# Kernel optimization log

Measured on AMD Instinct MI355X. Metric: run time of the kernel, lower is better.

Reference implementation:

```python
import jax, jax.numpy as jnp
import numpy as np

E = 300000        # num_edges
T = 3000000       # num_triplets
D = 128           # edge_message_dim
N_RAD = 6
N_SPH = 7
D_DOWN = 64       # edge_down_dim
D_BAS = 8         # basis_embed_dim


def _w(key, fan_in, fan_out):
    return jax.random.normal(key, (fan_in, fan_out), jnp.float32) / np.sqrt(fan_in)


def setup_inputs() -> dict:
    key = jax.random.key(0)
    ks = jax.random.split(key, 32)
    inp = {
        "x": jax.random.normal(ks[0], (E, D), jnp.float32),
        "rbf": jax.random.uniform(ks[1], (E, N_RAD), jnp.float32),
        "sbf": jax.random.uniform(ks[2], (T, N_SPH * N_RAD), jnp.float32),
        "idx_kj": jax.random.randint(ks[3], (T,), 0, E),
        "idx_ji": jax.random.randint(ks[4], (T,), 0, E),
        # basis projections (bias-free)
        "w_rbf1": _w(ks[5], N_RAD, D_BAS),
        "w_rbf2": _w(ks[6], D_BAS, D),
        "w_sbf1": _w(ks[7], N_SPH * N_RAD, D_BAS),
        "w_sbf2": _w(ks[8], D_BAS, D_DOWN),
        # message linears (with bias)
        "w_kj": _w(ks[9], D, D), "b_kj": jnp.zeros((D,), jnp.float32),
        "w_ji": _w(ks[10], D, D), "b_ji": jnp.zeros((D,), jnp.float32),
        # down / up projections (bias-free)
        "w_down": _w(ks[11], D, D_DOWN),
        "w_up": _w(ks[12], D_DOWN, D),
        # residual block before skip + dense
        "res1_w1": _w(ks[13], D, D), "res1_b1": jnp.zeros((D,), jnp.float32),
        "res1_w2": _w(ks[14], D, D), "res1_b2": jnp.zeros((D,), jnp.float32),
        "w_bs": _w(ks[15], D, D), "b_bs": jnp.zeros((D,), jnp.float32),
        # two residual blocks after skip
        "res2_w1": _w(ks[16], D, D), "res2_b1": jnp.zeros((D,), jnp.float32),
        "res2_w2": _w(ks[17], D, D), "res2_b2": jnp.zeros((D,), jnp.float32),
        "res3_w1": _w(ks[18], D, D), "res3_b1": jnp.zeros((D,), jnp.float32),
        "res3_w2": _w(ks[19], D, D), "res3_b2": jnp.zeros((D,), jnp.float32),
    }
    return inp


def _res_block(h, w1, b1, w2, b2):
    # h + act(lin2(act(lin1(h)))) with Swish(beta=1) == silu
    return h + jax.nn.silu(jax.nn.silu(h @ w1 + b1) @ w2 + b2)


def reference(x, rbf, sbf, idx_kj, idx_ji,
              w_rbf1, w_rbf2, w_sbf1, w_sbf2,
              w_kj, b_kj, w_ji, b_ji, w_down, w_up,
              res1_w1, res1_b1, res1_w2, res1_b2, w_bs, b_bs,
              res2_w1, res2_b1, res2_w2, res2_b2,
              res3_w1, res3_b1, res3_w2, res3_b2):
    act = jax.nn.silu
    x_ji = act(x @ w_ji + b_ji)                       # [E, D]
    x_kj = act(x @ w_kj + b_kj)                       # [E, D]
    rbf_e = (rbf @ w_rbf1) @ w_rbf2                   # [E, D]
    x_kj = act((x_kj * rbf_e) @ w_down)               # [E, D_DOWN]
    sbf_e = (sbf @ w_sbf1) @ w_sbf2                   # [T, D_DOWN]
    m = x_kj[idx_kj] * sbf_e                          # gather + Hadamard [T, D_DOWN]
    agg = jax.ops.segment_sum(m, idx_ji, num_segments=x.shape[0])  # [E, D_DOWN]
    x_kj = act(agg @ w_up)                            # [E, D]
    h = _res_block(x_ji + x_kj, res1_w1, res1_b1, res1_w2, res1_b2)
    h = act(h @ w_bs + b_bs) + x                      # skip connection
    h = _res_block(h, res2_w1, res2_b1, res2_w2, res2_b2)
    h = _res_block(h, res3_w1, res3_b1, res3_w2, res3_b2)
    return h
```

## Files before the change

### kernel.cpp

```cpp
#include <hip/hip_runtime.h>
#include <hip/hip_bf16.h>


typedef __attribute__((ext_vector_type(8))) _Float16 f16x8;
typedef __attribute__((ext_vector_type(4))) float f32x4;

__device__ __forceinline__ float silu_f(float v) {
    return v * __builtin_amdgcn_rcpf(1.0f + __expf(-v));
}

__device__ __forceinline__ void split44h(f32x4 a, f32x4 b, f16x8& hi, f16x8& lo) {
    float f[8] = {a[0], a[1], a[2], a[3], b[0], b[1], b[2], b[3]};
    #pragma unroll
    for (int j = 0; j < 8; ++j) {
        const _Float16 h = (_Float16)f[j];
        hi[j] = h;
        lo[j] = (_Float16)(f[j] - (float)h);
    }
}

__device__ __forceinline__ void gll16(const void* g, void* l) {
    __builtin_amdgcn_global_load_lds((const __attribute__((address_space(1))) void*)g,
                                     (__attribute__((address_space(3))) void*)l, 16, 0, 0);
}
__device__ __forceinline__ void stage8k(const char* g, _Float16* l, int lane, int wid) {
    #pragma unroll
    for (int i = 0; i < 2; ++i) {
        const int off = ((i * 4 + wid) << 10);
        gll16(g + off + lane * 16, (char*)l + off);
    }
}
__device__ __forceinline__ void stage4k(const char* g, _Float16* l, int lane, int wid) {
    const int off = (wid << 10);
    gll16(g + off + lane * 16, (char*)l + off);
}

template<int NF>
__device__ __forceinline__ void mfma_ks(f16x8 ah, f16x8 al, const _Float16* slot,
                                        int acol, int kq, f32x4* acc) {
    #pragma unroll
    for (int n = 0; n < NF; ++n) {
        const int c = n * 16 + acol;
        const int sw = (kq ^ ((c >> 1) & 3)) << 3;
        const f16x8 bh = *(const f16x8*)&slot[c * 32 + sw];
        acc[n] = __builtin_amdgcn_mfma_f32_16x16x32_f16(ah, bh, acc[n], 0, 0, 0);
        acc[n] = __builtin_amdgcn_mfma_f32_16x16x32_f16(al, bh, acc[n], 0, 0, 0);
    }
}

__device__ __forceinline__ void tfrag(const float* tl, int rb, int q, int kq,
                                      f16x8& Ah, f16x8& Al) {
    const f32x4 ta = *(const f32x4*)&tl[rb + q * 32 + kq * 8];
    const f32x4 tb = *(const f32x4*)&tl[rb + q * 32 + kq * 8 + 4];
    split44h(ta, tb, Ah, Al);
}

__device__ __forceinline__ void tgemm4(const char* img, const char* imgnext,
                                       _Float16* sA, _Float16* sB, const float* tl, int rb,
                                       int kq, int acol, int lane, int wid, f32x4* acc)
{
    f16x8 Ah[4], Al[4];
    #pragma unroll
    for (int q = 0; q < 4; ++q) tfrag(tl, rb, q, kq, Ah[q], Al[q]);

    stage8k(img + 8192, sB, lane, wid);
    mfma_ks<8>(Ah[0], Al[0], sA, acol, kq, acc); __syncthreads();
    stage8k(img + 16384, sA, lane, wid);
    mfma_ks<8>(Ah[1], Al[1], sB, acol, kq, acc); __syncthreads();
    stage8k(img + 24576, sB, lane, wid);
    mfma_ks<8>(Ah[2], Al[2], sA, acol, kq, acc); __syncthreads();
    if (imgnext) stage8k(imgnext, sA, lane, wid);
    mfma_ks<8>(Ah[3], Al[3], sB, acol, kq, acc); __syncthreads();
}

#define TPITCH 132

struct WDesc { const float* src; char* dst; int K; int N; };
struct WPrepArgs { WDesc w[11]; };

__global__ void wprep_kernel(WPrepArgs args) {
    const WDesc d = args.w[blockIdx.y];
    const int h = blockIdx.x;
    if (h * 32 >= d.K) return;
    char* slab = d.dst + (size_t)h * d.N * 64;
    for (int idx = threadIdx.x; idx < d.N * 4; idx += 256) {
        const int c = idx >> 2, ch = idx & 3;
        f16x8 v;
        #pragma unroll
        for (int j = 0; j < 8; ++j)
            v[j] = (_Float16)d.src[(size_t)(h * 32 + ch * 8 + j) * d.N + c];
        *(f16x8*)(slab + c * 64 + ((ch ^ ((c >> 1) & 3)) << 4)) = v;
    }
}


__global__ void rbf1_kernel(const float* __restrict__ rbf, const float* __restrict__ w_rbf1,
                            float* __restrict__ re1, int E) {
    const int i = blockIdx.x * 256 + threadIdx.x;
    const int e = i >> 3, p = i & 7;
    if (e < E) {
        float s = 0.f;
        #pragma unroll
        for (int q = 0; q < 6; ++q) s = fmaf(rbf[e * 6 + q], w_rbf1[q * 8 + p], s);
        re1[i] = s;
    }
}

__global__ void count_rank_kernel(const int* __restrict__ idx_ji, int* __restrict__ cnt,
                                  int* __restrict__ rank, int T) {
    const int i = (blockIdx.x * 256 + threadIdx.x) * 4;
    if (i + 3 < T) {
        const int4 j = *(const int4*)&idx_ji[i];
        int4 r;
        r.x = atomicAdd(&cnt[j.x], 1);
        r.y = atomicAdd(&cnt[j.y], 1);
        r.z = atomicAdd(&cnt[j.z], 1);
        r.w = atomicAdd(&cnt[j.w], 1);
        *(int4*)&rank[i] = r;
    } else {
        for (int k = i; k < T; ++k) rank[k] = atomicAdd(&cnt[idx_ji[k]], 1);
    }
}

__global__ void scan_partial_kernel(const int* __restrict__ cnt, int* __restrict__ partial, int E) {
    __shared__ int red[256];
    const int tid = threadIdx.x;
    const int base = blockIdx.x * 1024 + tid * 4;
    int s = 0;
    #pragma unroll
    for (int i = 0; i < 4; ++i) { const int g = base + i; if (g < E) s += cnt[g]; }
    red[tid] = s;
    __syncthreads();
    for (int off = 128; off > 0; off >>= 1) {
        if (tid < off) red[tid] += red[tid + off];
        __syncthreads();
    }
    if (tid == 0) partial[blockIdx.x] = red[0];
}

__global__ void scan_block_kernel(const int* __restrict__ partial, int* __restrict__ blockoff,
                                  int NB, int* offsets, int E) {
    __shared__ int red[256];
    const int tid = threadIdx.x;
    int v[4]; int s = 0;
    #pragma unroll
    for (int i = 0; i < 4; ++i) { const int g = tid * 4 + i; v[i] = (g < NB) ? partial[g] : 0; s += v[i]; }
    red[tid] = s;
    __syncthreads();
    for (int off = 1; off < 256; off <<= 1) {
        const int add = (tid >= off) ? red[tid - off] : 0;
        __syncthreads();
        red[tid] += add;
        __syncthreads();
    }
    int excl = (tid == 0) ? 0 : red[tid - 1];
    #pragma unroll
    for (int i = 0; i < 4; ++i) { const int g = tid * 4 + i; if (g < NB) blockoff[g] = excl; excl += v[i]; }
    if (tid == 255) offsets[E] = red[255];
}

__global__ void scan_final_kernel(const int* __restrict__ cnt, const int* __restrict__ blockoff,
                                  int* __restrict__ offsets, int E) {
    __shared__ int red[256];
    const int tid = threadIdx.x;
    const int base = blockIdx.x * 1024 + tid * 4;
    int v[4]; int s = 0;
    #pragma unroll
    for (int i = 0; i < 4; ++i) { const int g = base + i; v[i] = (g < E) ? cnt[g] : 0; s += v[i]; }
    red[tid] = s;
    __syncthreads();
    for (int off = 1; off < 256; off <<= 1) {
        const int add = (tid >= off) ? red[tid - off] : 0;
        __syncthreads();
        red[tid] += add;
        __syncthreads();
    }
    int run = blockoff[blockIdx.x] + ((tid == 0) ? 0 : red[tid - 1]);
    #pragma unroll
    for (int i = 0; i < 4; ++i) {
        const int g = base + i;
        if (g < E) offsets[g] = run;
        run += v[i];
    }
}

__launch_bounds__(256, 3)
__global__ void e1fill_kernel(const float* __restrict__ sbf, const float* __restrict__ w_sbf1,
                              const int* __restrict__ idx_ji, const int* __restrict__ idx_kj,
                              const int* __restrict__ rank, const int* __restrict__ offsets,
                              _Float16* __restrict__ E1p, int* __restrict__ kjp, int T)
{
    __shared__ float s_lds[256 * 43];
    const int tid = threadIdx.x;
    const long long t0 = (long long)blockIdx.x * 256;
    const int nrow = min(256, (int)(T - t0));
    const int nel  = nrow * 42;
    const float* base = sbf + t0 * 42;

    for (int i = tid * 4; i + 3 < nel; i += 1024) {
        const float4 v = *(const float4*)&base[i];
        s_lds[(i + 0) + (i + 0) / 42] = v.x;
        s_lds[(i + 1) + (i + 1) / 42] = v.y;
        s_lds[(i + 2) + (i + 2) / 42] = v.z;
        s_lds[(i + 3) + (i + 3) / 42] = v.w;
    }
    const int tail0 = nel & ~3;
    if (tid < nel - tail0) { const int g = tail0 + tid; s_lds[g + g / 42] = base[g]; }
    __syncthreads();

    const int t = (int)t0 + tid;
    if (t >= T) return;
    const float* srow = &s_lds[tid * 43];
    float e1[8] = {0.f, 0.f, 0.f, 0.f, 0.f, 0.f, 0.f, 0.f};
    #pragma unroll
    for (int q = 0; q < 42; ++q) {
        const float s = srow[q];
        #pragma unroll
        for (int p = 0; p < 8; ++p) e1[p] = fmaf(s, w_sbf1[q * 8 + p], e1[p]);
    }
    f16x8 eh;
    #pragma unroll
    for (int p = 0; p < 8; ++p) eh[p] = (_Float16)e1[p];
    const int ji  = idx_ji[t];
    const int pos = offsets[ji] + rank[t];
    *(f16x8*)&E1p[(size_t)pos * 8] = eh;
    kjp[pos] = idx_kj[t];
}

__launch_bounds__(256, 4)
__global__ void gather_kernel(const _Float16* __restrict__ E1p, const int* __restrict__ kjp,
                              const float* __restrict__ w_sbf2, const int* __restrict__ offsets,
                              const _Float16* __restrict__ xkjd, float* __restrict__ agg, int E)
{
    const int tid  = threadIdx.x;
    const int lane = tid & 63;
    const int e    = blockIdx.x * 4 + (tid >> 6);

    float w2[8];
    #pragma unroll
    for (int p = 0; p < 8; ++p) w2[p] = w_sbf2[p * 64 + lane];

    if (e >= E) return;
    const int j0 = __builtin_amdgcn_readfirstlane(offsets[e]);
    const int j1 = __builtin_amdgcn_readfirstlane(offsets[e + 1]);

    float acc = 0.f;
    if (j0 < j1) {
        int kj = __builtin_amdgcn_readfirstlane(kjp[j0]);
        f16x8 ev = *(const f16x8*)&E1p[(size_t)j0 * 8];
        float xv = (float)xkjd[(size_t)kj * 64 + lane];
        for (int j = j0; j < j1; ++j) {
            float xn = 0.f; f16x8 evn = {};
            if (j + 1 < j1) {
                const int kn = __builtin_amdgcn_readfirstlane(kjp[j + 1]);
                evn = *(const f16x8*)&E1p[(size_t)(j + 1) * 8];
                xn  = (float)xkjd[(size_t)kn * 64 + lane];
            }
            float sv = (float)ev[0] * w2[0];
            sv = fmaf((float)ev[1], w2[1], sv);
            sv = fmaf((float)ev[2], w2[2], sv);
            sv = fmaf((float)ev[3], w2[3], sv);
            sv = fmaf((float)ev[4], w2[4], sv);
            sv = fmaf((float)ev[5], w2[5], sv);
            sv = fmaf((float)ev[6], w2[6], sv);
            sv = fmaf((float)ev[7], w2[7], sv);
            acc = fmaf(xv, sv, acc);
            ev = evn; xv = xn;
        }
    }
    agg[(size_t)e * 64 + lane] = acc;
}

__launch_bounds__(256, 3)
__global__ void k1_kernel(const float* __restrict__ x, const char* __restrict__ wkj_i,
                          const float* __restrict__ b_kj, const float* __restrict__ re1,
                          const float* __restrict__ w_rbf2, const char* __restrict__ wdn_i,
                          _Float16* __restrict__ W3, int E)
{
    __shared__ _Float16 slotA[4096], slotB[4096];
    __shared__ float t_lds[64 * TPITCH];
    __shared__ float w2_lds[8 * 128];
    const int tid = threadIdx.x, lane = tid & 63, wid = tid >> 6;
    const int acol = lane & 15, kq = lane >> 4;
    const int rowW = blockIdx.x * 64 + wid * 16;
    const int arow = rowW + acol;
    const bool av = arow < E;

    stage8k(wkj_i, slotA, lane, wid);
    const float* xr = x + (size_t)arow * 128;
    f16x8 aH[4], aL[4];
    #pragma unroll
    for (int ks = 0; ks < 4; ++ks) {
        f32x4 a0 = f32x4{0.f, 0.f, 0.f, 0.f}, a1 = f32x4{0.f, 0.f, 0.f, 0.f};
        if (av) { a0 = *(const f32x4*)&xr[ks * 32 + kq * 8];
                  a1 = *(const f32x4*)&xr[ks * 32 + kq * 8 + 4]; }
        split44h(a0, a1, aH[ks], aL[ks]);
    }
    float bv[8];
    #pragma unroll
    for (int n = 0; n < 8; ++n) bv[n] = b_kj[n * 16 + acol];
    f32x4 e1a[4], e1b[4];
    #pragma unroll
    for (int r = 0; r < 4; ++r) {
        const int ge = rowW + kq * 4 + r;
        e1a[r] = f32x4{0.f, 0.f, 0.f, 0.f}; e1b[r] = f32x4{0.f, 0.f, 0.f, 0.f};
        if (ge < E) { e1a[r] = *(const f32x4*)&re1[(size_t)ge * 8];
                      e1b[r] = *(const f32x4*)&re1[(size_t)ge * 8 + 4]; }
    }
    for (int i = tid; i < 1024; i += 256) w2_lds[i] = w_rbf2[i];
    __syncthreads();

    f32x4 acc[8];
    #pragma unroll
    for (int n = 0; n < 8; ++n) acc[n] = f32x4{0.f, 0.f, 0.f, 0.f};

    stage8k(wkj_i + 8192, slotB, lane, wid);
    mfma_ks<8>(aH[0], aL[0], slotA, acol, kq, acc); __syncthreads();
    stage8k(wkj_i + 16384, slotA, lane, wid);
    mfma_ks<8>(aH[1], aL[1], slotB, acol, kq, acc); __syncthreads();
    stage8k(wkj_i + 24576, slotB, lane, wid);
    mfma_ks<8>(aH[2], aL[2], slotA, acol, kq, acc); __syncthreads();
    stage4k(wdn_i, slotA, lane, wid);
    mfma_ks<8>(aH[3], aL[3], slotB, acol, kq, acc); __syncthreads();

    #pragma unroll
    for (int n = 0; n < 8; ++n) {
        const int c = n * 16 + acol;
        float w2c[8];
        #pragma unroll
        for (int p = 0; p < 8; ++p) w2c[p] = w2_lds[p * 128 + c];
        #pragma unroll
        for (int r = 0; r < 4; ++r) {
            float s = e1a[r][0] * w2c[0];
            s = fmaf(e1a[r][1], w2c[1], s);
            s = fmaf(e1a[r][2], w2c[2], s);
            s = fmaf(e1a[r][3], w2c[3], s);
            s = fmaf(e1b[r][0], w2c[4], s);
            s = fmaf(e1b[r][1], w2c[5], s);
            s = fmaf(e1b[r][2], w2c[6], s);
            s = fmaf(e1b[r][3], w2c[7], s);
            t_lds[(wid * 16 + kq * 4 + r) * TPITCH + c] = silu_f(acc[n][r] + bv[n]) * s;
        }
    }
    __syncthreads();

    f32x4 acc2[4];
    #pragma unroll
    for (int n = 0; n < 4; ++n) acc2[n] = f32x4{0.f, 0.f, 0.f, 0.f};
    const int rb = (wid * 16 + acol) * TPITCH;

    f16x8 tH[4], tL[4];
    #pragma unroll
    for (int q = 0; q < 4; ++q) tfrag(t_lds, rb, q, kq, tH[q], tL[q]);

    stage4k(wdn_i + 4096, slotB, lane, wid);
    mfma_ks<4>(tH[0], tL[0], slotA, acol, kq, acc2); __syncthreads();
    stage4k(wdn_i + 8192, slotA, lane, wid);
    mfma_ks<4>(tH[1], tL[1], slotB, acol, kq, acc2); __syncthreads();
    stage4k(wdn_i + 12288, slotB, lane, wid);
    mfma_ks<4>(tH[2], tL[2], slotA, acol, kq, acc2); __syncthreads();
    mfma_ks<4>(tH[3], tL[3], slotB, acol, kq, acc2);

    #pragma unroll
    for (int n = 0; n < 4; ++n) {
        const int c = n * 16 + acol;
        #pragma unroll
        for (int r = 0; r < 4; ++r) {
            const int ge = rowW + kq * 4 + r;
            if (ge < E) W3[(size_t)ge * 64 + c] = (_Float16)silu_f(acc2[n][r]);
        }
    }
}

struct KBigArgs {
    const float* x; const float* W4; float* out;
    const char *wji, *wup, *r1w1, *r1w2, *wbs, *r2w1, *r2w2, *r3w1, *r3w2;
    const float *bji, *r1b1, *r1b2, *bbs, *r2b1, *r2b2, *r3b1, *r3b2;
    int E;
};

__launch_bounds__(256, 3)
__global__ void kbig_kernel(KBigArgs A_)
{
    __shared__ _Float16 slotA[4096], slotB[4096];
    __shared__ float t_lds[64 * TPITCH];
    const int tid = threadIdx.x, lane = tid & 63, wid = tid >> 6;
    const int acol = lane & 15, kq = lane >> 4;
    const int rowW = blockIdx.x * 64 + wid * 16;
    const int arow = rowW + acol;
    const int E = A_.E;
    const bool av = arow < E;
    const int rb = (wid * 16 + acol) * TPITCH;

    stage8k(A_.wji, slotA, lane, wid);

    const float* xr = A_.x + (size_t)arow * 128;
    const float* wr = A_.W4 + (size_t)arow * 64;
    f16x8 aH[4], aL[4], uH[2], uL[2];
    #pragma unroll
    for (int ks = 0; ks < 4; ++ks) {
        f32x4 a0 = f32x4{0.f, 0.f, 0.f, 0.f}, a1 = f32x4{0.f, 0.f, 0.f, 0.f};
        if (av) { a0 = *(const f32x4*)&xr[ks * 32 + kq * 8];
                  a1 = *(const f32x4*)&xr[ks * 32 + kq * 8 + 4]; }
        split44h(a0, a1, aH[ks], aL[ks]);
    }
    #pragma unroll
    for (int ks = 0; ks < 2; ++ks) {
        f32x4 u0 = f32x4{0.f, 0.f, 0.f, 0.f}, u1 = f32x4{0.f, 0.f, 0.f, 0.f};
        if (av) { u0 = *(const f32x4*)&wr[ks * 32 + kq * 8];
                  u1 = *(const f32x4*)&wr[ks * 32 + kq * 8 + 4]; }
        split44h(u0, u1, uH[ks], uL[ks]);
    }
    __syncthreads();

    f32x4 acc[8];
    #pragma unroll
    for (int n = 0; n < 8; ++n) acc[n] = f32x4{0.f, 0.f, 0.f, 0.f};

    stage8k(A_.wji + 8192, slotB, lane, wid);
    mfma_ks<8>(aH[0], aL[0], slotA, acol, kq, acc); __syncthreads();
    stage8k(A_.wji + 16384, slotA, lane, wid);
    mfma_ks<8>(aH[1], aL[1], slotB, acol, kq, acc); __syncthreads();
    stage8k(A_.wji + 24576, slotB, lane, wid);
    mfma_ks<8>(aH[2], aL[2], slotA, acol, kq, acc); __syncthreads();
    stage8k(A_.wup, slotA, lane, wid);
    mfma_ks<8>(aH[3], aL[3], slotB, acol, kq, acc); __syncthreads();

    float res[8][4];
    #pragma unroll
    for (int n = 0; n < 8; ++n) {
        const float bv = A_.bji[n * 16 + acol];
        #pragma unroll
        for (int r = 0; r < 4; ++r) { res[n][r] = silu_f(acc[n][r] + bv); acc[n][r] = 0.f; }
    }

    stage8k(A_.wup + 8192, slotB, lane, wid);
    mfma_ks<8>(uH[0], uL[0], slotA, acol, kq, acc); __syncthreads();
    stage8k(A_.r1w1, slotA, lane, wid);
    mfma_ks<8>(uH[1], uL[1], slotB, acol, kq, acc); __syncthreads();

    #pragma unroll
    for (int n = 0; n < 8; ++n) {
        const int c = n * 16 + acol;
        #pragma unroll
        for (int r = 0; r < 4; ++r) {
            res[n][r] += silu_f(acc[n][r]);
            t_lds[(wid * 16 + kq * 4 + r) * TPITCH + c] = res[n][r];
            acc[n][r] = 0.f;
        }
    }
    __syncthreads();

    tgemm4(A_.r1w1, A_.r1w2, slotA, slotB, t_lds, rb, kq, acol, lane, wid, acc);
    #pragma unroll
    for (int n = 0; n < 8; ++n) {
        const float bv = A_.r1b1[n * 16 + acol];
        const int c = n * 16 + acol;
        #pragma unroll
        for (int r = 0; r < 4; ++r) {
            t_lds[(wid * 16 + kq * 4 + r) * TPITCH + c] = silu_f(acc[n][r] + bv);
            acc[n][r] = 0.f;
        }
    }
    __syncthreads();

    tgemm4(A_.r1w2, A_.wbs, slotA, slotB, t_lds, rb, kq, acol, lane, wid, acc);
    #pragma unroll
    for (int n = 0; n < 8; ++n) {
        const float bv = A_.r1b2[n * 16 + acol];
        const int c = n * 16 + acol;
        #pragma unroll
        for (int r = 0; r < 4; ++r) {
            t_lds[(wid * 16 + kq * 4 + r) * TPITCH + c] = res[n][r] + silu_f(acc[n][r] + bv);
            acc[n][r] = 0.f;
        }
    }
    __syncthreads();

    tgemm4(A_.wbs, A_.r2w1, slotA, slotB, t_lds, rb, kq, acol, lane, wid, acc);
    #pragma unroll
    for (int n = 0; n < 8; ++n) {
        const float bv = A_.bbs[n * 16 + acol];
        const int c = n * 16 + acol;
        #pragma unroll
        for (int r = 0; r < 4; ++r) {
            const int ge = rowW + kq * 4 + r;
            const float xv = (ge < E) ? A_.x[(size_t)ge * 128 + c] : 0.f;
            res[n][r] = silu_f(acc[n][r] + bv) + xv;
            t_lds[(wid * 16 + kq * 4 + r) * TPITCH + c] = res[n][r];
            acc[n][r] = 0.f;
        }
    }
    __syncthreads();

    tgemm4(A_.r2w1, A_.r2w2, slotA, slotB, t_lds, rb, kq, acol, lane, wid, acc);
    #pragma unroll
    for (int n = 0; n < 8; ++n) {
        const float bv = A_.r2b1[n * 16 + acol];
        const int c = n * 16 + acol;
        #pragma unroll
        for (int r = 0; r < 4; ++r) {
            t_lds[(wid * 16 + kq * 4 + r) * TPITCH + c] = silu_f(acc[n][r] + bv);
            acc[n][r] = 0.f;
        }
    }
    __syncthreads();

    tgemm4(A_.r2w2, A_.r3w1, slotA, slotB, t_lds, rb, kq, acol, lane, wid, acc);
    #pragma unroll
    for (int n = 0; n < 8; ++n) {
        const float bv = A_.r2b2[n * 16 + acol];
        const int c = n * 16 + acol;
        #pragma unroll
        for (int r = 0; r < 4; ++r) {
            res[n][r] += silu_f(acc[n][r] + bv);
            t_lds[(wid * 16 + kq * 4 + r) * TPITCH + c] = res[n][r];
            acc[n][r] = 0.f;
        }
    }
    __syncthreads();

    tgemm4(A_.r3w1, A_.r3w2, slotA, slotB, t_lds, rb, kq, acol, lane, wid, acc);
    #pragma unroll
    for (int n = 0; n < 8; ++n) {
        const float bv = A_.r3b1[n * 16 + acol];
        const int c = n * 16 + acol;
        #pragma unroll
        for (int r = 0; r < 4; ++r) {
            t_lds[(wid * 16 + kq * 4 + r) * TPITCH + c] = silu_f(acc[n][r] + bv);
            acc[n][r] = 0.f;
        }
    }
    __syncthreads();

    tgemm4(A_.r3w2, nullptr, slotA, slotB, t_lds, rb, kq, acol, lane, wid, acc);
    #pragma unroll
    for (int n = 0; n < 8; ++n) {
        const float bv = A_.r3b2[n * 16 + acol];
        const int c = n * 16 + acol;
        #pragma unroll
        for (int r = 0; r < 4; ++r) {
            const int ge = rowW + kq * 4 + r;
            if (ge < E)
                A_.out[(size_t)ge * 128 + c] = res[n][r] + silu_f(acc[n][r] + bv);
        }
    }
}


extern "C" void kernel_launch(void* const* d_in, const int* in_sizes, int n_in,
                              void* d_out, int out_size, void* d_ws, size_t ws_size,
                              hipStream_t stream)
{
    const float* x      = (const float*)d_in[0];
    const float* rbf    = (const float*)d_in[1];
    const float* sbf    = (const float*)d_in[2];
    const int*   idx_kj = (const int*)d_in[3];
    const int*   idx_ji = (const int*)d_in[4];
    const float* w_rbf1 = (const float*)d_in[5];
    const float* w_rbf2 = (const float*)d_in[6];
    const float* w_sbf1 = (const float*)d_in[7];
    const float* w_sbf2 = (const float*)d_in[8];
    const float* w_kj   = (const float*)d_in[9];
    const float* b_kj   = (const float*)d_in[10];
    const float* w_ji   = (const float*)d_in[11];
    const float* b_ji   = (const float*)d_in[12];
    const float* w_down = (const float*)d_in[13];
    const float* w_up   = (const float*)d_in[14];
    const float* r1w1   = (const float*)d_in[15];
    const float* r1b1   = (const float*)d_in[16];
    const float* r1w2   = (const float*)d_in[17];
    const float* r1b2   = (const float*)d_in[18];
    const float* w_bs   = (const float*)d_in[19];
    const float* b_bs   = (const float*)d_in[20];
    const float* r2w1   = (const float*)d_in[21];
    const float* r2b1   = (const float*)d_in[22];
    const float* r2w2   = (const float*)d_in[23];
    const float* r2b2   = (const float*)d_in[24];
    const float* r3w1   = (const float*)d_in[25];
    const float* r3b1   = (const float*)d_in[26];
    const float* r3w2   = (const float*)d_in[27];
    const float* r3b2   = (const float*)d_in[28];

    const int E = in_sizes[0] / 128;
    const int T = in_sizes[2] / 42;

    float* OUT = (float*)d_out;
    _Float16* W3 = (_Float16*)((char*)d_ws + (size_t)E * 128 * 4);
    float* W4  = (float*)((char*)d_ws + (size_t)E * 128 * 4
                                      + (size_t)E * 64 * 4);

    int*   cnt      = (int*)d_ws;
    int*   offsets  = cnt + (E + 64);
    int*   partial  = offsets + (E + 64);
    int*   blockoff = partial + 1024;
    _Float16* E1p   = (_Float16*)((char*)d_ws + (4u << 20));
    int*   kjp      = (int*)((char*)d_ws + (102u << 20));
    float* re1      = (float*)((char*)d_ws + (116u << 20));
    char*  wimg     = (char*)d_ws + (130u << 20);
    int*   rank     = (int*)((char*)d_ws + (134u << 20));

    char* wkj_i  = wimg;
    char* wji_i  = wimg + 32768;
    char* wdn_i  = wimg + 65536;
    char* wup_i  = wimg + 81920;
    char* r1w1_i = wimg + 98304;
    char* r1w2_i = wimg + 131072;
    char* wbs_i  = wimg + 163840;
    char* r2w1_i = wimg + 196608;
    char* r2w2_i = wimg + 229376;
    char* r3w1_i = wimg + 262144;
    char* r3w2_i = wimg + 294912;

    WPrepArgs pa;
    pa.w[0]  = {w_kj,   wkj_i,  128, 128};
    pa.w[1]  = {w_ji,   wji_i,  128, 128};
    pa.w[2]  = {w_down, wdn_i,  128,  64};
    pa.w[3]  = {w_up,   wup_i,   64, 128};
    pa.w[4]  = {r1w1,   r1w1_i, 128, 128};
    pa.w[5]  = {r1w2,   r1w2_i, 128, 128};
    pa.w[6]  = {w_bs,   wbs_i,  128, 128};
    pa.w[7]  = {r2w1,   r2w1_i, 128, 128};
    pa.w[8]  = {r2w2,   r2w2_i, 128, 128};
    pa.w[9]  = {r3w1,   r3w1_i, 128, 128};
    pa.w[10] = {r3w2,   r3w2_i, 128, 128};

    const dim3 b256(256);
    const int gB  = (E + 63) / 64;
    const int gT  = (T + 255) / 256;
    const int gT4 = (T + 1023) / 1024;
    const int NB  = (E + 1023) / 1024;
    const int gE4 = (E + 3) / 4;
    const int gR  = (E * 8 + 255) / 256;

    wprep_kernel<<<dim3(4, 11), b256, 0, stream>>>(pa);
    rbf1_kernel<<<gR, b256, 0, stream>>>(rbf, w_rbf1, re1, E);
    hipMemsetAsync(cnt, 0, (size_t)E * 4, stream);
    count_rank_kernel<<<gT4, b256, 0, stream>>>(idx_ji, cnt, rank, T);
    scan_partial_kernel<<<NB, b256, 0, stream>>>(cnt, partial, E);
    scan_block_kernel<<<1, b256, 0, stream>>>(partial, blockoff, NB, offsets, E);
    scan_final_kernel<<<NB, b256, 0, stream>>>(cnt, blockoff, offsets, E);
    e1fill_kernel<<<gT, b256, 0, stream>>>(sbf, w_sbf1, idx_ji, idx_kj, rank, offsets, E1p, kjp, T);

    k1_kernel<<<gB, b256, 0, stream>>>(x, wkj_i, b_kj, re1, w_rbf2, wdn_i, W3, E);
    gather_kernel<<<gE4, b256, 0, stream>>>(E1p, kjp, w_sbf2, offsets, W3, W4, E);

    KBigArgs ka;
    ka.x = x; ka.W4 = W4; ka.out = OUT;
    ka.wji = wji_i; ka.wup = wup_i; ka.r1w1 = r1w1_i; ka.r1w2 = r1w2_i; ka.wbs = wbs_i;
    ka.r2w1 = r2w1_i; ka.r2w2 = r2w2_i; ka.r3w1 = r3w1_i; ka.r3w2 = r3w2_i;
    ka.bji = b_ji; ka.r1b1 = r1b1; ka.r1b2 = r1b2; ka.bbs = b_bs;
    ka.r2b1 = r2b1; ka.r2b2 = r2b2; ka.r3b1 = r3b1; ka.r3b2 = r3b2;
    ka.E = E;
    kbig_kernel<<<gB, b256, 0, stream>>>(ka);
}
```

Baseline: 999.0 us.

## Merge independent prologue kernels and co-schedule k1 with e1fill in one launch

```diff
diff --git a/kernel.cpp b/kernel.cpp
--- a/kernel.cpp
+++ b/kernel.cpp
@@ -74,13 +74,19 @@
 }
 
 #define TPITCH 132
+#define SMEM_K1 54272
 
 struct WDesc { const float* src; char* dst; int K; int N; };
-struct WPrepArgs { WDesc w[11]; };
-
-__global__ void wprep_kernel(WPrepArgs args) {
-    const WDesc d = args.w[blockIdx.y];
-    const int h = blockIdx.x;
+struct ProArgs {
+    WDesc w[11];
+    const float* rbf; const float* w_rbf1; float* re1; int E;
+    const int* idx_ji; int* cnt; int* rank; int T;
+    int nW, nR;
+};
+
+__device__ void wprep_body(const ProArgs& P, int b) {
+    const WDesc d = P.w[b >> 2];
+    const int h = b & 3;
     if (h * 32 >= d.K) return;
     char* slab = d.dst + (size_t)h * d.N * 64;
     for (int idx = threadIdx.x; idx < d.N * 4; idx += 256) {
@@ -93,34 +99,40 @@
     }
 }
 
-
-__global__ void rbf1_kernel(const float* __restrict__ rbf, const float* __restrict__ w_rbf1,
-                            float* __restrict__ re1, int E) {
-    const int i = blockIdx.x * 256 + threadIdx.x;
+__device__ void rbf1_body(const ProArgs& P, int b) {
+    const int i = b * 256 + threadIdx.x;
     const int e = i >> 3, p = i & 7;
-    if (e < E) {
+    if (e < P.E) {
         float s = 0.f;
         #pragma unroll
-        for (int q = 0; q < 6; ++q) s = fmaf(rbf[e * 6 + q], w_rbf1[q * 8 + p], s);
-        re1[i] = s;
-    }
-}
-
-__global__ void count_rank_kernel(const int* __restrict__ idx_ji, int* __restrict__ cnt,
-                                  int* __restrict__ rank, int T) {
-    const int i = (blockIdx.x * 256 + threadIdx.x) * 4;
+        for (int q = 0; q < 6; ++q) s = fmaf(P.rbf[e * 6 + q], P.w_rbf1[q * 8 + p], s);
+        P.re1[i] = s;
+    }
+}
+
+__device__ void count_rank_body(const ProArgs& P, int b) {
+    const int i = (b * 256 + threadIdx.x) * 4;
+    const int T = P.T;
     if (i + 3 < T) {
-        const int4 j = *(const int4*)&idx_ji[i];
+        const int4 j = *(const int4*)&P.idx_ji[i];
         int4 r;
-        r.x = atomicAdd(&cnt[j.x], 1);
-        r.y = atomicAdd(&cnt[j.y], 1);
-        r.z = atomicAdd(&cnt[j.z], 1);
-        r.w = atomicAdd(&cnt[j.w], 1);
-        *(int4*)&rank[i] = r;
+        r.x = atomicAdd(&P.cnt[j.x], 1);
+        r.y = atomicAdd(&P.cnt[j.y], 1);
+        r.z = atomicAdd(&P.cnt[j.z], 1);
+        r.w = atomicAdd(&P.cnt[j.w], 1);
+        *(int4*)&P.rank[i] = r;
     } else {
-        for (int k = i; k < T; ++k) rank[k] = atomicAdd(&cnt[idx_ji[k]], 1);
-    }
-}
+        for (int k = i; k < T; ++k) P.rank[k] = atomicAdd(&P.cnt[P.idx_ji[k]], 1);
+    }
+}
+
+__global__ void pro_kernel(ProArgs P) {
+    const int b = blockIdx.x;
+    if (b < P.nW)            wprep_body(P, b);
+    else if (b < P.nW + P.nR) rbf1_body(P, b - P.nW);
+    else                      count_rank_body(P, b - P.nW - P.nR);
+}
+
 
 __global__ void scan_partial_kernel(const int* __restrict__ cnt, int* __restrict__ partial, int E) {
     __shared__ int red[256];
@@ -184,18 +196,120 @@
     }
 }
 
-__launch_bounds__(256, 3)
-__global__ void e1fill_kernel(const float* __restrict__ sbf, const float* __restrict__ w_sbf1,
-                              const int* __restrict__ idx_ji, const int* __restrict__ idx_kj,
-                              const int* __restrict__ rank, const int* __restrict__ offsets,
-                              _Float16* __restrict__ E1p, int* __restrict__ kjp, int T)
-{
-    __shared__ float s_lds[256 * 43];
+struct K1E1Args {
+    const float* x; const char* wkj_i; const float* b_kj; const float* re1;
+    const float* w_rbf2; const char* wdn_i; _Float16* W3; int E; int gB;
+    const float* sbf; const float* w_sbf1;
+    const int* idx_ji; const int* idx_kj; const int* rank; const int* offsets;
+    _Float16* E1p; int* kjp; int T;
+};
+
+__device__ void k1_body(char* smem, int bx, const K1E1Args& A) {
+    _Float16* slotA = (_Float16*)smem;
+    _Float16* slotB = (_Float16*)(smem + 8192);
+    float* t_lds    = (float*)(smem + 16384);
+    float* w2_lds   = (float*)(smem + 16384 + 64 * TPITCH * 4);
+    const int tid = threadIdx.x, lane = tid & 63, wid = tid >> 6;
+    const int acol = lane & 15, kq = lane >> 4;
+    const int rowW = bx * 64 + wid * 16;
+    const int arow = rowW + acol;
+    const int E = A.E;
+    const bool av = arow < E;
+
+    stage8k(A.wkj_i, slotA, lane, wid);
+    const float* xr = A.x + (size_t)arow * 128;
+    f16x8 aH[4], aL[4];
+    #pragma unroll
+    for (int ks = 0; ks < 4; ++ks) {
+        f32x4 a0 = f32x4{0.f, 0.f, 0.f, 0.f}, a1 = f32x4{0.f, 0.f, 0.f, 0.f};
+        if (av) { a0 = *(const f32x4*)&xr[ks * 32 + kq * 8];
+                  a1 = *(const f32x4*)&xr[ks * 32 + kq * 8 + 4]; }
+        split44h(a0, a1, aH[ks], aL[ks]);
+    }
+    float bv[8];
+    #pragma unroll
+    for (int n = 0; n < 8; ++n) bv[n] = A.b_kj[n * 16 + acol];
+    f32x4 e1a[4], e1b[4];
+    #pragma unroll
+    for (int r = 0; r < 4; ++r) {
+        const int ge = rowW + kq * 4 + r;
+        e1a[r] = f32x4{0.f, 0.f, 0.f, 0.f}; e1b[r] = f32x4{0.f, 0.f, 0.f, 0.f};
+        if (ge < E) { e1a[r] = *(const f32x4*)&A.re1[(size_t)ge * 8];
+                      e1b[r] = *(const f32x4*)&A.re1[(size_t)ge * 8 + 4]; }
+    }
+    for (int i = tid; i < 1024; i += 256) w2_lds[i] = A.w_rbf2[i];
+    __syncthreads();
+
+    f32x4 acc[8];
+    #pragma unroll
+    for (int n = 0; n < 8; ++n) acc[n] = f32x4{0.f, 0.f, 0.f, 0.f};
+
+    stage8k(A.wkj_i + 8192, slotB, lane, wid);
+    mfma_ks<8>(aH[0], aL[0], slotA, acol, kq, acc); __syncthreads();
+    stage8k(A.wkj_i + 16384, slotA, lane, wid);
+    mfma_ks<8>(aH[1], aL[1], slotB, acol, kq, acc); __syncthreads();
+    stage8k(A.wkj_i + 24576, slotB, lane, wid);
+    mfma_ks<8>(aH[2], aL[2], slotA, acol, kq, acc); __syncthreads();
+    stage4k(A.wdn_i, slotA, lane, wid);
+    mfma_ks<8>(aH[3], aL[3], slotB, acol, kq, acc); __syncthreads();
+
+    #pragma unroll
+    for (int n = 0; n < 8; ++n) {
+        const int c = n * 16 + acol;
+        float w2c[8];
+        #pragma unroll
+        for (int p = 0; p < 8; ++p) w2c[p] = w2_lds[p * 128 + c];
+        #pragma unroll
+        for (int r = 0; r < 4; ++r) {
+            float s = e1a[r][0] * w2c[0];
+            s = fmaf(e1a[r][1], w2c[1], s);
+            s = fmaf(e1a[r][2], w2c[2], s);
+            s = fmaf(e1a[r][3], w2c[3], s);
+            s = fmaf(e1b[r][0], w2c[4], s);
+            s = fmaf(e1b[r][1], w2c[5], s);
+            s = fmaf(e1b[r][2], w2c[6], s);
+            s = fmaf(e1b[r][3], w2c[7], s);
+            t_lds[(wid * 16 + kq * 4 + r) * TPITCH + c] = silu_f(acc[n][r] + bv[n]) * s;
+        }
+    }
+    __syncthreads();
+
+    f32x4 acc2[4];
+    #pragma unroll
+    for (int n = 0; n < 4; ++n) acc2[n] = f32x4{0.f, 0.f, 0.f, 0.f};
+    const int rb = (wid * 16 + acol) * TPITCH;
+
+    f16x8 tH[4], tL[4];
+    #pragma unroll
+    for (int q = 0; q < 4; ++q) tfrag(t_lds, rb, q, kq, tH[q], tL[q]);
+
+    stage4k(A.wdn_i + 4096, slotB, lane, wid);
+    mfma_ks<4>(tH[0], tL[0], slotA, acol, kq, acc2); __syncthreads();
+    stage4k(A.wdn_i + 8192, slotA, lane, wid);
+    mfma_ks<4>(tH[1], tL[1], slotB, acol, kq, acc2); __syncthreads();
+    stage4k(A.wdn_i + 12288, slotB, lane, wid);
+    mfma_ks<4>(tH[2], tL[2], slotA, acol, kq, acc2); __syncthreads();
+    mfma_ks<4>(tH[3], tL[3], slotB, acol, kq, acc2);
+
+    #pragma unroll
+    for (int n = 0; n < 4; ++n) {
+        const int c = n * 16 + acol;
+        #pragma unroll
+        for (int r = 0; r < 4; ++r) {
+            const int ge = rowW + kq * 4 + r;
+            if (ge < E) A.W3[(size_t)ge * 64 + c] = (_Float16)silu_f(acc2[n][r]);
+        }
+    }
+}
+
+__device__ void e1fill_body(char* smem, int bx, const K1E1Args& A) {
+    float* s_lds = (float*)smem;
     const int tid = threadIdx.x;
-    const long long t0 = (long long)blockIdx.x * 256;
+    const int T = A.T;
+    const long long t0 = (long long)bx * 256;
     const int nrow = min(256, (int)(T - t0));
     const int nel  = nrow * 42;
-    const float* base = sbf + t0 * 42;
+    const float* base = A.sbf + t0 * 42;
 
     for (int i = tid * 4; i + 3 < nel; i += 1024) {
         const float4 v = *(const float4*)&base[i];
@@ -216,15 +330,23 @@
     for (int q = 0; q < 42; ++q) {
         const float s = srow[q];
         #pragma unroll
-        for (int p = 0; p < 8; ++p) e1[p] = fmaf(s, w_sbf1[q * 8 + p], e1[p]);
+        for (int p = 0; p < 8; ++p) e1[p] = fmaf(s, A.w_sbf1[q * 8 + p], e1[p]);
     }
     f16x8 eh;
     #pragma unroll
     for (int p = 0; p < 8; ++p) eh[p] = (_Float16)e1[p];
-    const int ji  = idx_ji[t];
-    const int pos = offsets[ji] + rank[t];
-    *(f16x8*)&E1p[(size_t)pos * 8] = eh;
-    kjp[pos] = idx_kj[t];
+    const int ji  = A.idx_ji[t];
+    const int pos = A.offsets[ji] + A.rank[t];
+    *(f16x8*)&A.E1p[(size_t)pos * 8] = eh;
+    A.kjp[pos] = A.idx_kj[t];
+}
+
+__launch_bounds__(256, 2)
+__global__ void k1e1_kernel(K1E1Args A) {
+    __shared__ __align__(16) char smem[SMEM_K1];
+    const int b = blockIdx.x;
+    if (b < A.gB) k1_body(smem, b, A);
+    else          e1fill_body(smem, b - A.gB, A);
 }
 
 __launch_bounds__(256, 4)
@@ -269,107 +391,6 @@
         }
     }
     agg[(size_t)e * 64 + lane] = acc;
-}
-
-__launch_bounds__(256, 3)
-__global__ void k1_kernel(const float* __restrict__ x, const char* __restrict__ wkj_i,
-                          const float* __restrict__ b_kj, const float* __restrict__ re1,
-                          const float* __restrict__ w_rbf2, const char* __restrict__ wdn_i,
-                          _Float16* __restrict__ W3, int E)
-{
-    __shared__ _Float16 slotA[4096], slotB[4096];
-    __shared__ float t_lds[64 * TPITCH];
-    __shared__ float w2_lds[8 * 128];
-    const int tid = threadIdx.x, lane = tid & 63, wid = tid >> 6;
-    const int acol = lane & 15, kq = lane >> 4;
-    const int rowW = blockIdx.x * 64 + wid * 16;
-    const int arow = rowW + acol;
-    const bool av = arow < E;
-
-    stage8k(wkj_i, slotA, lane, wid);
-    const float* xr = x + (size_t)arow * 128;
-    f16x8 aH[4], aL[4];
-    #pragma unroll
-    for (int ks = 0; ks < 4; ++ks) {
-        f32x4 a0 = f32x4{0.f, 0.f, 0.f, 0.f}, a1 = f32x4{0.f, 0.f, 0.f, 0.f};
-        if (av) { a0 = *(const f32x4*)&xr[ks * 32 + kq * 8];
-                  a1 = *(const f32x4*)&xr[ks * 32 + kq * 8 + 4]; }
-        split44h(a0, a1, aH[ks], aL[ks]);
-    }
-    float bv[8];
-    #pragma unroll
-    for (int n = 0; n < 8; ++n) bv[n] = b_kj[n * 16 + acol];
-    f32x4 e1a[4], e1b[4];
-    #pragma unroll
-    for (int r = 0; r < 4; ++r) {
-        const int ge = rowW + kq * 4 + r;
-        e1a[r] = f32x4{0.f, 0.f, 0.f, 0.f}; e1b[r] = f32x4{0.f, 0.f, 0.f, 0.f};
-        if (ge < E) { e1a[r] = *(const f32x4*)&re1[(size_t)ge * 8];
-                      e1b[r] = *(const f32x4*)&re1[(size_t)ge * 8 + 4]; }
-    }
-    for (int i = tid; i < 1024; i += 256) w2_lds[i] = w_rbf2[i];
-    __syncthreads();
-
-    f32x4 acc[8];
-    #pragma unroll
-    for (int n = 0; n < 8; ++n) acc[n] = f32x4{0.f, 0.f, 0.f, 0.f};
-
-    stage8k(wkj_i + 8192, slotB, lane, wid);
-    mfma_ks<8>(aH[0], aL[0], slotA, acol, kq, acc); __syncthreads();
-    stage8k(wkj_i + 16384, slotA, lane, wid);
-    mfma_ks<8>(aH[1], aL[1], slotB, acol, kq, acc); __syncthreads();
-    stage8k(wkj_i + 24576, slotB, lane, wid);
-    mfma_ks<8>(aH[2], aL[2], slotA, acol, kq, acc); __syncthreads();
-    stage4k(wdn_i, slotA, lane, wid);
-    mfma_ks<8>(aH[3], aL[3], slotB, acol, kq, acc); __syncthreads();
-
-    #pragma unroll
-    for (int n = 0; n < 8; ++n) {
-        const int c = n * 16 + acol;
-        float w2c[8];
-        #pragma unroll
-        for (int p = 0; p < 8; ++p) w2c[p] = w2_lds[p * 128 + c];
-        #pragma unroll
-        for (int r = 0; r < 4; ++r) {
-            float s = e1a[r][0] * w2c[0];
-            s = fmaf(e1a[r][1], w2c[1], s);
-            s = fmaf(e1a[r][2], w2c[2], s);
-            s = fmaf(e1a[r][3], w2c[3], s);
-            s = fmaf(e1b[r][0], w2c[4], s);
-            s = fmaf(e1b[r][1], w2c[5], s);
-            s = fmaf(e1b[r][2], w2c[6], s);
-            s = fmaf(e1b[r][3], w2c[7], s);
-            t_lds[(wid * 16 + kq * 4 + r) * TPITCH + c] = silu_f(acc[n][r] + bv[n]) * s;
-        }
-    }
-    __syncthreads();
-
-    f32x4 acc2[4];
-    #pragma unroll
-    for (int n = 0; n < 4; ++n) acc2[n] = f32x4{0.f, 0.f, 0.f, 0.f};
-    const int rb = (wid * 16 + acol) * TPITCH;
-
-    f16x8 tH[4], tL[4];
-    #pragma unroll
-    for (int q = 0; q < 4; ++q) tfrag(t_lds, rb, q, kq, tH[q], tL[q]);
-
-    stage4k(wdn_i + 4096, slotB, lane, wid);
-    mfma_ks<4>(tH[0], tL[0], slotA, acol, kq, acc2); __syncthreads();
-    stage4k(wdn_i + 8192, slotA, lane, wid);
-    mfma_ks<4>(tH[1], tL[1], slotB, acol, kq, acc2); __syncthreads();
-    stage4k(wdn_i + 12288, slotB, lane, wid);
-    mfma_ks<4>(tH[2], tL[2], slotA, acol, kq, acc2); __syncthreads();
-    mfma_ks<4>(tH[3], tL[3], slotB, acol, kq, acc2);
-
-    #pragma unroll
-    for (int n = 0; n < 4; ++n) {
-        const int c = n * 16 + acol;
-        #pragma unroll
-        for (int r = 0; r < 4; ++r) {
-            const int ge = rowW + kq * 4 + r;
-            if (ge < E) W3[(size_t)ge * 64 + c] = (_Float16)silu_f(acc2[n][r]);
-        }
-    }
 }
 
 struct KBigArgs {
@@ -612,19 +633,6 @@
     char* r3w1_i = wimg + 262144;
     char* r3w2_i = wimg + 294912;
 
-    WPrepArgs pa;
-    pa.w[0]  = {w_kj,   wkj_i,  128, 128};
-    pa.w[1]  = {w_ji,   wji_i,  128, 128};
-    pa.w[2]  = {w_down, wdn_i,  128,  64};
-    pa.w[3]  = {w_up,   wup_i,   64, 128};
-    pa.w[4]  = {r1w1,   r1w1_i, 128, 128};
-    pa.w[5]  = {r1w2,   r1w2_i, 128, 128};
-    pa.w[6]  = {w_bs,   wbs_i,  128, 128};
-    pa.w[7]  = {r2w1,   r2w1_i, 128, 128};
-    pa.w[8]  = {r2w2,   r2w2_i, 128, 128};
-    pa.w[9]  = {r3w1,   r3w1_i, 128, 128};
-    pa.w[10] = {r3w2,   r3w2_i, 128, 128};
-
     const dim3 b256(256);
     const int gB  = (E + 63) / 64;
     const int gT  = (T + 255) / 256;
@@ -633,16 +641,36 @@
     const int gE4 = (E + 3) / 4;
     const int gR  = (E * 8 + 255) / 256;
 
-    wprep_kernel<<<dim3(4, 11), b256, 0, stream>>>(pa);
-    rbf1_kernel<<<gR, b256, 0, stream>>>(rbf, w_rbf1, re1, E);
+    ProArgs P;
+    P.w[0]  = {w_kj,   wkj_i,  128, 128};
+    P.w[1]  = {w_ji,   wji_i,  128, 128};
+    P.w[2]  = {w_down, wdn_i,  128,  64};
+    P.w[3]  = {w_up,   wup_i,   64, 128};
+    P.w[4]  = {r1w1,   r1w1_i, 128, 128};
+    P.w[5]  = {r1w2,   r1w2_i, 128, 128};
+    P.w[6]  = {w_bs,   wbs_i,  128, 128};
+    P.w[7]  = {r2w1,   r2w1_i, 128, 128};
+    P.w[8]  = {r2w2,   r2w2_i, 128, 128};
+    P.w[9]  = {r3w1,   r3w1_i, 128, 128};
+    P.w[10] = {r3w2,   r3w2_i, 128, 128};
+    P.rbf = rbf; P.w_rbf1 = w_rbf1; P.re1 = re1; P.E = E;
+    P.idx_ji = idx_ji; P.cnt = cnt; P.rank = rank; P.T = T;
+    P.nW = 44; P.nR = gR;
+
     hipMemsetAsync(cnt, 0, (size_t)E * 4, stream);
-    count_rank_kernel<<<gT4, b256, 0, stream>>>(idx_ji, cnt, rank, T);
+    pro_kernel<<<44 + gR + gT4, b256, 0, stream>>>(P);
     scan_partial_kernel<<<NB, b256, 0, stream>>>(cnt, partial, E);
     scan_block_kernel<<<1, b256, 0, stream>>>(partial, blockoff, NB, offsets, E);
     scan_final_kernel<<<NB, b256, 0, stream>>>(cnt, blockoff, offsets, E);
-    e1fill_kernel<<<gT, b256, 0, stream>>>(sbf, w_sbf1, idx_ji, idx_kj, rank, offsets, E1p, kjp, T);
-
-    k1_kernel<<<gB, b256, 0, stream>>>(x, wkj_i, b_kj, re1, w_rbf2, wdn_i, W3, E);
+
+    K1E1Args KA;
+    KA.x = x; KA.wkj_i = wkj_i; KA.b_kj = b_kj; KA.re1 = re1;
+    KA.w_rbf2 = w_rbf2; KA.wdn_i = wdn_i; KA.W3 = W3; KA.E = E; KA.gB = gB;
+    KA.sbf = sbf; KA.w_sbf1 = w_sbf1;
+    KA.idx_ji = idx_ji; KA.idx_kj = idx_kj; KA.rank = rank; KA.offsets = offsets;
+    KA.E1p = E1p; KA.kjp = kjp; KA.T = T;
+    k1e1_kernel<<<gB + gT, b256, 0, stream>>>(KA);
+
     gather_kernel<<<gE4, b256, 0, stream>>>(E1p, kjp, w_sbf2, offsets, W3, W4, E);
 
     KBigArgs ka;
```

Result: slower. 1.068 ms (+6.9%).
